# Optimization experiments

Measured on AMD Instinct MI355X. Metric: run time of the kernel, lower is better.

The kernel has to match this reference:

```python
import jax, jax.numpy as jnp
import numpy as np

N = 50000        # nodes
E = 1_600_000    # edges
F_IN = 128       # input feature dim
EMB = 48         # emb_size
HID = 48         # hidden_size
OUT = 64         # out_sizes[0]
K = 7            # Chebyshev order


def setup_inputs() -> dict:
    key = jax.random.key(0)
    ks = jax.random.split(key, 8)
    x = jax.random.normal(ks[0], (N, F_IN), dtype=jnp.float32)
    edge_index = jax.random.randint(ks[1], (2, E), 0, N, dtype=jnp.int32)
    edge_weight = jax.random.uniform(ks[2], (E,), dtype=jnp.float32)
    W_in = jax.random.normal(ks[3], (F_IN, EMB), jnp.float32) / np.float32(np.sqrt(F_IN))
    b_in = jnp.zeros((EMB,), jnp.float32)
    W_cheb = jax.random.normal(ks[4], (K, EMB, HID), jnp.float32) / np.float32(np.sqrt(EMB))
    b_cheb = jnp.zeros((HID,), jnp.float32)
    W_out = jax.random.normal(ks[5], (HID, OUT), jnp.float32) / np.float32(np.sqrt(HID))
    b_out = jnp.zeros((OUT,), jnp.float32)
    return dict(x=x, edge_index=edge_index, edge_weight=edge_weight,
                W_in=W_in, b_in=b_in, W_cheb=W_cheb, b_cheb=b_cheb,
                W_out=W_out, b_out=b_out)


def reference(x, edge_index, edge_weight, W_in, b_in, W_cheb, b_cheb, W_out, b_out):
    row, col = edge_index[0], edge_index[1]
    # PyG ChebConv sym normalization with lambda_max=2:
    #   L_hat = 2/lambda_max * (I - D^-1/2 A D^-1/2) - I = -D^-1/2 A D^-1/2
    deg = jax.ops.segment_sum(edge_weight, row, num_segments=N)
    dinv = jnp.where(deg > 0, jax.lax.rsqrt(deg), 0.0)
    norm = -dinv[row] * edge_weight * dinv[col]  # [E]

    # input Linear + ReLU (Dropout is identity at eval)
    xf = jax.nn.relu(x @ W_in + b_in)  # [N, EMB]

    def prop(t):
        # out[i] = sum_{(j->i) in E} norm_e * t[j]
        return jax.ops.segment_sum(norm[:, None] * t[row], col, num_segments=N)

    # Chebyshev recursion: T0 = x, T1 = L_hat x, T_k = 2 L_hat T_{k-1} - T_{k-2}
    Tx0 = xf
    out = Tx0 @ W_cheb[0]
    Tx1 = prop(Tx0)
    out = out + Tx1 @ W_cheb[1]
    for k in range(2, K):
        Tx2 = 2.0 * prop(Tx1) - Tx0
        out = out + Tx2 @ W_cheb[k]
        Tx0, Tx1 = Tx1, Tx2
    out = out + b_cheb

    y = jax.nn.relu(out)          # ReLU after ChebConv (out_drop = identity at eval)
    y = y @ W_out + b_out          # output Linear
    return (y, xf)
```

## Files before the change

### kernel.cpp

```cpp
#include <hip/hip_runtime.h>
#include <hip/hip_fp16.h>

#define N_NODES 50000
#define N_EDGES 1600000
#define F_IN    128
#define EMB     48
#define HID     48
#define OUTF    64
#define KCH     7
#define TPAD    64

#define NR    8
#define RANGE (N_NODES / NR)
#define BPR   64
#define SLICE (N_EDGES / BPR)
#define HTHREADS 512
#define NBLK  ((N_NODES + 255) / 256)
#define NTILES (N_NODES / 16)

typedef __attribute__((ext_vector_type(8))) _Float16 half8;
typedef __attribute__((ext_vector_type(4))) float f32x4;

#define PROP_GATHER_LOOP(TSRC)                                                  \
    {                                                                           \
        int e16 = s + ((e - s) & ~15);                                          \
        for (; p < e16; p += 16) {                                              \
            float ww[16]; uint2 hv[16];                                         \
            _Pragma("unroll")                                                   \
            for (int j = 0; j < 16; ++j) {                                      \
                uint2 er = edges[p + j];                                        \
                ww[j] = __uint_as_float(er.y);                                  \
                hv[j] = *reinterpret_cast<const uint2*>(                        \
                    TSRC + (size_t)er.x * TPAD + 4 * lane);                     \
            }                                                                   \
            _Pragma("unroll")                                                   \
            for (int j = 0; j < 16; ++j) {                                      \
                __half2 h01 = *reinterpret_cast<__half2*>(&hv[j].x);            \
                __half2 h23 = *reinterpret_cast<__half2*>(&hv[j].y);            \
                a0 += ww[j] * __low2float(h01);                                 \
                a1 += ww[j] * __high2float(h01);                                \
                a2 += ww[j] * __low2float(h23);                                 \
                a3 += ww[j] * __high2float(h23);                                \
            }                                                                   \
        }                                                                       \
        int e4b = p + ((e - p) & ~3);                                           \
        for (; p < e4b; p += 4) {                                               \
            float ww[4]; uint2 hv[4];                                           \
            _Pragma("unroll")                                                   \
            for (int j = 0; j < 4; ++j) {                                       \
                uint2 er = edges[p + j];                                        \
                ww[j] = __uint_as_float(er.y);                                  \
                hv[j] = *reinterpret_cast<const uint2*>(                        \
                    TSRC + (size_t)er.x * TPAD + 4 * lane);                     \
            }                                                                   \
            _Pragma("unroll")                                                   \
            for (int j = 0; j < 4; ++j) {                                       \
                __half2 h01 = *reinterpret_cast<__half2*>(&hv[j].x);            \
                __half2 h23 = *reinterpret_cast<__half2*>(&hv[j].y);            \
                a0 += ww[j] * __low2float(h01);                                 \
                a1 += ww[j] * __high2float(h01);                                \
                a2 += ww[j] * __low2float(h23);                                 \
                a3 += ww[j] * __high2float(h23);                                \
            }                                                                   \
        }                                                                       \
        for (; p < e; ++p) {                                                    \
            uint2 er = edges[p];                                                \
            float wv = __uint_as_float(er.y);                                   \
            uint2 hv = *reinterpret_cast<const uint2*>(                         \
                TSRC + (size_t)er.x * TPAD + 4 * lane);                         \
            __half2 h01 = *reinterpret_cast<__half2*>(&hv.x);                   \
            __half2 h23 = *reinterpret_cast<__half2*>(&hv.y);                   \
            a0 += wv * __low2float(h01);                                        \
            a1 += wv * __high2float(h01);                                       \
            a2 += wv * __low2float(h23);                                        \
            a3 += wv * __high2float(h23);                                       \
        }                                                                       \
    }

__global__ __launch_bounds__(HTHREADS) void hist_part_kernel(
    const int* __restrict__ row, const int* __restrict__ col,
    const float* __restrict__ w,
    unsigned short* __restrict__ pc, float* __restrict__ pd)
{
    __shared__ unsigned lc32[RANGE / 2];
    __shared__ float    ld[RANGE];
    int t = threadIdx.x;
    for (int i = t; i < RANGE / 2; i += HTHREADS) lc32[i] = 0u;
    for (int i = t; i < RANGE; i += HTHREADS) ld[i] = 0.f;
    __syncthreads();
    int r = blockIdx.x / BPR;
    int b = blockIdx.x % BPR;
    int base = r * RANGE;
    int lo = b * SLICE;
    for (int e0 = lo + t * 4; e0 < lo + SLICE; e0 += HTHREADS * 4) {
        int4   c4 = *(const int4*)&col[e0];
        int4   r4 = *(const int4*)&row[e0];
        float4 w4 = *(const float4*)&w[e0];
        int ci, ri;
        ci = c4.x - base; if ((unsigned)ci < RANGE) atomicAdd(&lc32[ci >> 1], 1u << ((ci & 1) * 16));
        ri = r4.x - base; if ((unsigned)ri < RANGE) atomicAdd(&ld[ri], w4.x);
        ci = c4.y - base; if ((unsigned)ci < RANGE) atomicAdd(&lc32[ci >> 1], 1u << ((ci & 1) * 16));
        ri = r4.y - base; if ((unsigned)ri < RANGE) atomicAdd(&ld[ri], w4.y);
        ci = c4.z - base; if ((unsigned)ci < RANGE) atomicAdd(&lc32[ci >> 1], 1u << ((ci & 1) * 16));
        ri = r4.z - base; if ((unsigned)ri < RANGE) atomicAdd(&ld[ri], w4.z);
        ci = c4.w - base; if ((unsigned)ci < RANGE) atomicAdd(&lc32[ci >> 1], 1u << ((ci & 1) * 16));
        ri = r4.w - base; if ((unsigned)ri < RANGE) atomicAdd(&ld[ri], w4.w);
    }
    __syncthreads();
    unsigned short* pcb = pc + (size_t)blockIdx.x * RANGE;
    float*          pdb = pd + (size_t)blockIdx.x * RANGE;
    for (int i = t; i < RANGE; i += HTHREADS) {
        pcb[i] = (unsigned short)((lc32[i >> 1] >> ((i & 1) * 16)) & 0xFFFFu);
        pdb[i] = ld[i];
    }
}

__global__ __launch_bounds__(256) void reduce_kernel(
    unsigned short* __restrict__ pc, const float* __restrict__ pd,
    float* __restrict__ dinv, int* __restrict__ off, int* __restrict__ bsum)
{
    int t = threadIdx.x;
    int n = blockIdx.x * 256 + t;
    int c = 0; float d = 0.f;
    if (n < N_NODES) {
        int r = n / RANGE, i = n - r * RANGE;
        size_t base = (size_t)r * BPR * RANGE + i;
        unsigned csum = 0;
        for (int b = 0; b < BPR; ++b) {
            size_t idx = base + (size_t)b * RANGE;
            unsigned x = pc[idx];
            pc[idx] = (unsigned short)csum;
            csum += x;
            d += pd[idx];
        }
        c = (int)csum;
        dinv[n] = d > 0.f ? rsqrtf(d) : 0.f;
    }
    int lane = t & 63, wid = t >> 6;
    int v = c;
    for (int s = 1; s < 64; s <<= 1) {
        int u = __shfl_up(v, s);
        if (lane >= s) v += u;
    }
    __shared__ int ws[4];
    if (lane == 63) ws[wid] = v;
    __syncthreads();
    int wb = 0;
    for (int i = 0; i < 4; ++i) if (i < wid) wb += ws[i];
    int ex = (v - c) + wb;
    if (n < N_NODES) off[n] = ex;
    if (t == 255) bsum[blockIdx.x] = ex + c;
}

__global__ __launch_bounds__(256) void bsum_scan_kernel(
    int* __restrict__ bsum, int* __restrict__ off)
{
    int t = threadIdx.x;
    int orig = (t < NBLK) ? bsum[t] : 0;
    int lane = t & 63, wid = t >> 6;
    int v = orig;
    for (int s = 1; s < 64; s <<= 1) {
        int u = __shfl_up(v, s);
        if (lane >= s) v += u;
    }
    __shared__ int ws[4];
    if (lane == 63) ws[wid] = v;
    __syncthreads();
    int wb = 0;
    for (int i = 0; i < 4; ++i) if (i < wid) wb += ws[i];
    int ex = (v - orig) + wb;
    if (t < NBLK) bsum[t] = ex;
    if (t == NBLK - 1) off[N_NODES] = ex + orig;
}

__global__ __launch_bounds__(256) void add_off_kernel(
    int* __restrict__ off, const int* __restrict__ bsum)
{
    int n = blockIdx.x * 256 + threadIdx.x;
    if (n < N_NODES) off[n] += bsum[n >> 8];
}

__global__ __launch_bounds__(HTHREADS) void scatter_part_kernel(
    const int* __restrict__ row, const int* __restrict__ col,
    const float* __restrict__ w, const float* __restrict__ dinv,
    const int* __restrict__ off, const unsigned short* __restrict__ pc,
    uint2* __restrict__ edges)
{
    __shared__ unsigned lc32[RANGE / 2];
    int t = threadIdx.x;
    for (int i = t; i < RANGE / 2; i += HTHREADS) lc32[i] = 0u;
    __syncthreads();
    int r = blockIdx.x / BPR;
    int b = blockIdx.x % BPR;
    int base = r * RANGE;
    int lo = b * SLICE;
    const unsigned short* pcb = pc + (size_t)blockIdx.x * RANGE;
    for (int e0 = lo + t * 4; e0 < lo + SLICE; e0 += HTHREADS * 4) {
        int4   c4 = *(const int4*)&col[e0];
        int4   r4 = *(const int4*)&row[e0];
        float4 w4 = *(const float4*)&w[e0];
        #pragma unroll
        for (int j = 0; j < 4; ++j) {
            int c  = (j == 0) ? c4.x : (j == 1) ? c4.y : (j == 2) ? c4.z : c4.w;
            int rw = (j == 0) ? r4.x : (j == 1) ? r4.y : (j == 2) ? r4.z : r4.w;
            float we = (j == 0) ? w4.x : (j == 1) ? w4.y : (j == 2) ? w4.z : w4.w;
            int ci = c - base;
            if ((unsigned)ci < RANGE) {
                unsigned old = atomicAdd(&lc32[ci >> 1], 1u << ((ci & 1) * 16));
                unsigned lrank = (old >> ((ci & 1) * 16)) & 0xFFFFu;
                float nr = -dinv[rw] * we * dinv[c];
                int pos = off[c] + (int)pcb[ci] + (int)lrank;
                edges[pos] = make_uint2((unsigned)rw, __float_as_uint(nr));
            }
        }
    }
}

__global__ __launch_bounds__(256) void xf_mfma_kernel(
    const float* __restrict__ x, const float* __restrict__ Win,
    const float* __restrict__ bin, float* __restrict__ xf_out,
    __half* __restrict__ T0h)
{
    __shared__ half8 Wf[3][4][64];
    __shared__ float bs[EMB];
    int t = threadIdx.x;
    for (int idx = t; idx < 3 * 4 * 64; idx += 256) {
        int j = idx >> 8;
        int rem = idx & 255;
        int s = rem >> 6;
        int l = rem & 63;
        int colw = j * 16 + (l & 15);
        int k0 = s * 32 + (l >> 4) * 8;
        half8 v;
        #pragma unroll
        for (int i = 0; i < 8; ++i)
            v[i] = (_Float16)Win[(k0 + i) * EMB + colw];
        Wf[j][s][l] = v;
    }
    if (t < EMB) bs[t] = bin[t];
    __syncthreads();

    int wid = t >> 6, lane = t & 63;
    int nt = blockIdx.x * 4 + wid;
    if (nt >= NTILES) return;
    int n0 = nt * 16;
    int arow = lane & 15, kg = lane >> 4;

    const float* xr = x + (size_t)(n0 + arow) * F_IN + kg * 8;
    half8 a[4];
    #pragma unroll
    for (int s = 0; s < 4; ++s) {
        f32x4 lo = *reinterpret_cast<const f32x4*>(xr + s * 32);
        f32x4 hi = *reinterpret_cast<const f32x4*>(xr + s * 32 + 4);
        half8 av;
        av[0] = (_Float16)lo[0]; av[1] = (_Float16)lo[1];
        av[2] = (_Float16)lo[2]; av[3] = (_Float16)lo[3];
        av[4] = (_Float16)hi[0]; av[5] = (_Float16)hi[1];
        av[6] = (_Float16)hi[2]; av[7] = (_Float16)hi[3];
        a[s] = av;
    }

    f32x4 c0 = {0.f, 0.f, 0.f, 0.f}, c1 = c0, c2 = c0;
    #pragma unroll
    for (int s = 0; s < 4; ++s) {
        c0 = __builtin_amdgcn_mfma_f32_16x16x32_f16(a[s], Wf[0][s][lane], c0, 0, 0, 0);
        c1 = __builtin_amdgcn_mfma_f32_16x16x32_f16(a[s], Wf[1][s][lane], c1, 0, 0, 0);
        c2 = __builtin_amdgcn_mfma_f32_16x16x32_f16(a[s], Wf[2][s][lane], c2, 0, 0, 0);
    }

    int ccol = lane & 15;
    #pragma unroll
    for (int j = 0; j < 3; ++j) {
        int colg = j * 16 + ccol;
        float bias = bs[colg];
        f32x4 cj = (j == 0) ? c0 : (j == 1) ? c1 : c2;
        #pragma unroll
        for (int r = 0; r < 4; ++r) {
            int n = n0 + kg * 4 + r;
            float v = fmaxf(cj[r] + bias, 0.f);
            xf_out[(size_t)n * EMB + colg] = v;
            T0h[(size_t)n * TPAD + colg] = __float2half_rn(v);
        }
    }
    {
        int n = n0 + (lane >> 2);
        int cp = 48 + (lane & 3) * 4;
        *reinterpret_cast<uint2*>(T0h + (size_t)n * TPAD + cp) = make_uint2(0u, 0u);
    }
}

__global__ __launch_bounds__(256) void prop_k1_kernel(
    const int* __restrict__ off, const uint2* __restrict__ edges,
    const __half* __restrict__ T0, __half* __restrict__ T1,
    const float* __restrict__ W0, const float* __restrict__ W1,
    float* __restrict__ out_acc)
{
    __shared__ float W0s[EMB * HID];
    __shared__ float W1s[EMB * HID];
    __shared__ float tdS[16][EMB + 1];
    __shared__ float t0S[16][EMB + 1];
    int t = threadIdx.x;
    for (int i = t; i < EMB * HID; i += 256) { W0s[i] = W0[i]; W1s[i] = W1[i]; }
    __syncthreads();

    int grp = t >> 4, lane = t & 15;
    int g = blockIdx.x * 16 + grp;

    float a0 = 0.f, a1 = 0.f, a2 = 0.f, a3 = 0.f;
    if (lane < 12) {
        int s = off[g], e = off[g + 1];
        int p = s;
        PROP_GATHER_LOOP(T0)
        uint2 tv = *reinterpret_cast<const uint2*>(T0 + (size_t)g * TPAD + 4 * lane);
        __half2 t01 = *reinterpret_cast<__half2*>(&tv.x);
        __half2 t23 = *reinterpret_cast<__half2*>(&tv.y);
        t0S[grp][4 * lane]     = __low2float(t01);
        t0S[grp][4 * lane + 1] = __high2float(t01);
        t0S[grp][4 * lane + 2] = __low2float(t23);
        t0S[grp][4 * lane + 3] = __high2float(t23);
        tdS[grp][4 * lane]     = a0;
        tdS[grp][4 * lane + 1] = a1;
        tdS[grp][4 * lane + 2] = a2;
        tdS[grp][4 * lane + 3] = a3;
    }
    {
        __half2 h01, h23;
        h01.x = __float2half_rn(a0); h01.y = __float2half_rn(a1);
        h23.x = __float2half_rn(a2); h23.y = __float2half_rn(a3);
        uint2 ov;
        ov.x = *reinterpret_cast<unsigned*>(&h01);
        ov.y = *reinterpret_cast<unsigned*>(&h23);
        *reinterpret_cast<uint2*>(T1 + (size_t)g * TPAD + 4 * lane) = ov;
    }

    float o0 = 0.f, o1 = 0.f, o2 = 0.f;
#pragma unroll 8
    for (int c = 0; c < EMB; ++c) {
        float t1v = tdS[grp][c];
        float t0v = t0S[grp][c];
        o0 += t1v * W1s[c * HID + lane]      + t0v * W0s[c * HID + lane];
        o1 += t1v * W1s[c * HID + lane + 16] + t0v * W0s[c * HID + lane + 16];
        o2 += t1v * W1s[c * HID + lane + 32] + t0v * W0s[c * HID + lane + 32];
    }
    float* orow = out_acc + (size_t)g * HID;
    orow[lane]      = o0;
    orow[lane + 16] = o1;
    orow[lane + 32] = o2;
}

__global__ __launch_bounds__(256) void prop_fused_kernel(
    const int* __restrict__ off, const uint2* __restrict__ edges,
    const __half* __restrict__ tsrc, const __half* __restrict__ tprev,
    __half* __restrict__ tdst, const float* __restrict__ Wk,
    float* __restrict__ out_acc)
{
    __shared__ float Ws[EMB * HID];
    __shared__ float tdS[16][EMB + 1];
    int t = threadIdx.x;
    for (int i = t; i < EMB * HID; i += 256) Ws[i] = Wk[i];
    __syncthreads();

    int grp = t >> 4, lane = t & 15;
    int g = blockIdx.x * 16 + grp;

    float a0 = 0.f, a1 = 0.f, a2 = 0.f, a3 = 0.f;
    if (lane < 12) {
        int s = off[g], e = off[g + 1];
        int p = s;
        PROP_GATHER_LOOP(tsrc)
        uint2 tv = *reinterpret_cast<const uint2*>(tprev + (size_t)g * TPAD + 4 * lane);
        __half2 t01 = *reinterpret_cast<__half2*>(&tv.x);
        __half2 t23 = *reinterpret_cast<__half2*>(&tv.y);
        a0 = 2.f * a0 - __low2float(t01);
        a1 = 2.f * a1 - __high2float(t01);
        a2 = 2.f * a2 - __low2float(t23);
        a3 = 2.f * a3 - __high2float(t23);
        tdS[grp][4 * lane]     = a0;
        tdS[grp][4 * lane + 1] = a1;
        tdS[grp][4 * lane + 2] = a2;
        tdS[grp][4 * lane + 3] = a3;
    }
    {
        __half2 h01, h23;
        h01.x = __float2half_rn(a0); h01.y = __float2half_rn(a1);
        h23.x = __float2half_rn(a2); h23.y = __float2half_rn(a3);
        uint2 ov;
        ov.x = *reinterpret_cast<unsigned*>(&h01);
        ov.y = *reinterpret_cast<unsigned*>(&h23);
        *reinterpret_cast<uint2*>(tdst + (size_t)g * TPAD + 4 * lane) = ov;
    }

    float o0 = 0.f, o1 = 0.f, o2 = 0.f;
#pragma unroll 8
    for (int c = 0; c < EMB; ++c) {
        float tv = tdS[grp][c];
        o0 += tv * Ws[c * HID + lane];
        o1 += tv * Ws[c * HID + lane + 16];
        o2 += tv * Ws[c * HID + lane + 32];
    }
    float* orow = out_acc + (size_t)g * HID;
    orow[lane]      += o0;
    orow[lane + 16] += o1;
    orow[lane + 32] += o2;
}

__global__ __launch_bounds__(256) void prop_final_kernel(
    const int* __restrict__ off, const uint2* __restrict__ edges,
    const __half* __restrict__ tsrc, const __half* __restrict__ tprev,
    const float* __restrict__ Wk, const float* __restrict__ out_acc,
    const float* __restrict__ bch, const float* __restrict__ Wout,
    const float* __restrict__ bout, float* __restrict__ y)
{
    __shared__ float Ws[EMB * HID];
    __shared__ float Wo[HID * OUTF];
    __shared__ float tdS[16][EMB + 1];
    __shared__ float vS[16][HID + 1];
    __shared__ float bchS[HID];
    __shared__ float boS[OUTF];
    int t = threadIdx.x;
    for (int i = t; i < EMB * HID; i += 256) Ws[i] = Wk[i];
    for (int i = t; i < HID * OUTF; i += 256) Wo[i] = Wout[i];
    if (t < HID) bchS[t] = bch[t];
    if (t < OUTF) boS[t] = bout[t];
    __syncthreads();

    int grp = t >> 4, lane = t & 15;
    int g = blockIdx.x * 16 + grp;

    float a0 = 0.f, a1 = 0.f, a2 = 0.f, a3 = 0.f;
    if (lane < 12) {
        int s = off[g], e = off[g + 1];
        int p = s;
        PROP_GATHER_LOOP(tsrc)
        uint2 tv = *reinterpret_cast<const uint2*>(tprev + (size_t)g * TPAD + 4 * lane);
        __half2 t01 = *reinterpret_cast<__half2*>(&tv.x);
        __half2 t23 = *reinterpret_cast<__half2*>(&tv.y);
        a0 = 2.f * a0 - __low2float(t01);
        a1 = 2.f * a1 - __high2float(t01);
        a2 = 2.f * a2 - __low2float(t23);
        a3 = 2.f * a3 - __high2float(t23);
        tdS[grp][4 * lane]     = a0;
        tdS[grp][4 * lane + 1] = a1;
        tdS[grp][4 * lane + 2] = a2;
        tdS[grp][4 * lane + 3] = a3;
    }

    float o0 = 0.f, o1 = 0.f, o2 = 0.f;
#pragma unroll 8
    for (int c = 0; c < EMB; ++c) {
        float tv = tdS[grp][c];
        o0 += tv * Ws[c * HID + lane];
        o1 += tv * Ws[c * HID + lane + 16];
        o2 += tv * Ws[c * HID + lane + 32];
    }
    const float* orow = out_acc + (size_t)g * HID;
    vS[grp][lane]      = fmaxf(orow[lane]      + o0 + bchS[lane],      0.f);
    vS[grp][lane + 16] = fmaxf(orow[lane + 16] + o1 + bchS[lane + 16], 0.f);
    vS[grp][lane + 32] = fmaxf(orow[lane + 32] + o2 + bchS[lane + 32], 0.f);

    float y0 = boS[4 * lane], y1 = boS[4 * lane + 1];
    float y2 = boS[4 * lane + 2], y3 = boS[4 * lane + 3];
#pragma unroll 8
    for (int h = 0; h < HID; ++h) {
        float v = vS[grp][h];
        float4 w4 = *reinterpret_cast<const float4*>(&Wo[h * OUTF + 4 * lane]);
        y0 += v * w4.x; y1 += v * w4.y; y2 += v * w4.z; y3 += v * w4.w;
    }
    *reinterpret_cast<float4*>(y + (size_t)g * OUTF + 4 * lane) =
        make_float4(y0, y1, y2, y3);
}

extern "C" void kernel_launch(void* const* d_in, const int* in_sizes, int n_in,
                              void* d_out, int out_size, void* d_ws, size_t ws_size,
                              hipStream_t stream)
{
    const float* x    = (const float*)d_in[0];
    const int*   ei   = (const int*)d_in[1];
    const float* ew   = (const float*)d_in[2];
    const float* Win  = (const float*)d_in[3];
    const float* bin  = (const float*)d_in[4];
    const float* Wch  = (const float*)d_in[5];
    const float* bch  = (const float*)d_in[6];
    const float* Wout = (const float*)d_in[7];
    const float* bout = (const float*)d_in[8];

    const int* row = ei;
    const int* col = ei + N_EDGES;

    float* y_out  = (float*)d_out;
    float* xf_out = (float*)d_out + (size_t)N_NODES * OUTF;

    char* p = (char*)d_ws;
    auto carve = [&](size_t bytes) {
        void* q = p;
        p += (bytes + 255) & ~(size_t)255;
        return q;
    };
    unsigned short* pc = (unsigned short*)carve((size_t)NR * BPR * RANGE * 2);
    float*    pd  = (float*)carve((size_t)NR * BPR * RANGE * 4);
    float*    dinv = (float*)carve(N_NODES * 4);
    int*      off  = (int*)  carve((N_NODES + 1) * 4);
    int*      bsum = (int*)  carve(NBLK * 4);
    uint2*    edges = (uint2*)carve((size_t)N_EDGES * 8);
    float*    out_acc = (float*)carve((size_t)N_NODES * HID * 4);
    __half*   T0h = (__half*)carve((size_t)N_NODES * TPAD * 2);
    __half*   TAh = (__half*)carve((size_t)N_NODES * TPAD * 2);
    __half*   TBh = (__half*)carve((size_t)N_NODES * TPAD * 2);
    __half*   TCh = (__half*)carve((size_t)N_NODES * TPAD * 2);

    hist_part_kernel<<<NR * BPR, HTHREADS, 0, stream>>>(row, col, ew, pc, pd);
    reduce_kernel<<<NBLK, 256, 0, stream>>>(pc, pd, dinv, off, bsum);
    bsum_scan_kernel<<<1, 256, 0, stream>>>(bsum, off);
    add_off_kernel<<<NBLK, 256, 0, stream>>>(off, bsum);
    scatter_part_kernel<<<NR * BPR, HTHREADS, 0, stream>>>(row, col, ew, dinv, off, pc, edges);

    xf_mfma_kernel<<<(NTILES + 3) / 4, 256, 0, stream>>>(x, Win, bin, xf_out, T0h);

    const int prop_grid = NTILES;

    prop_k1_kernel<<<prop_grid, 256, 0, stream>>>(off, edges, T0h, TAh,
                                                  Wch, Wch + EMB * HID, out_acc);
    const __half* A = T0h;
    __half*       B = TAh;
    __half* bufs[3] = {TBh, TCh, TAh};
    for (int k = 2; k < KCH - 1; ++k) {
        __half* C = bufs[(k - 2) % 3];
        prop_fused_kernel<<<prop_grid, 256, 0, stream>>>(off, edges, B, A,
                                                         C, Wch + (size_t)k * EMB * HID, out_acc);
        A = B; B = C;
    }
    prop_final_kernel<<<prop_grid, 256, 0, stream>>>(off, edges, B, A,
                                                     Wch + (size_t)(KCH - 1) * EMB * HID,
                                                     out_acc, bch, Wout, bout, y_out);
}
```

Baseline: 338.7 us.

## Pre-partition edges by source-node range before histogram and CSR scatter

Adds a three-kernel stable partition (count, scan, scatter) that reorders edges into 7 buckets by row>>13 before the existing histogram and CSR-building kernels run. The intent is to make later degree and scatter accesses to the per-row arrays more local, improving cache behaviour. In exchange it adds an extra full pass over the edge arrays, with writes to new row/col/weight buffers and strided scattered stores, plus three extra launches.

```diff
diff --git a/kernel.cpp b/kernel.cpp
--- a/kernel.cpp
+++ b/kernel.cpp
@@ -17,6 +17,12 @@
 #define HTHREADS 512
 #define NBLK  ((N_NODES + 255) / 256)
 #define NTILES (N_NODES / 16)
+
+#define SRSH  13
+#define NSR   7
+#define PNB   256
+#define PNT   256
+#define PTOT  (PNB * PNT)
 
 typedef __attribute__((ext_vector_type(8))) _Float16 half8;
 typedef __attribute__((ext_vector_type(4))) float f32x4;
@@ -77,6 +83,128 @@
         }                                                                       \
     }
 
+__global__ __launch_bounds__(PNT) void part_count_kernel(
+    const int* __restrict__ row, int* __restrict__ bsum7)
+{
+    __shared__ int cnt[NSR];
+    int t = threadIdx.x;
+    if (t < NSR) cnt[t] = 0;
+    __syncthreads();
+    int tid = blockIdx.x * PNT + t;
+    int c0 = 0, c1 = 0, c2 = 0, c3 = 0, c4 = 0, c5 = 0, c6 = 0;
+    for (int i = tid; i < N_EDGES; i += PTOT) {
+        int b = row[i] >> SRSH;
+        c0 += (b == 0); c1 += (b == 1); c2 += (b == 2); c3 += (b == 3);
+        c4 += (b == 4); c5 += (b == 5); c6 += (b == 6);
+    }
+    if (c0) atomicAdd(&cnt[0], c0);
+    if (c1) atomicAdd(&cnt[1], c1);
+    if (c2) atomicAdd(&cnt[2], c2);
+    if (c3) atomicAdd(&cnt[3], c3);
+    if (c4) atomicAdd(&cnt[4], c4);
+    if (c5) atomicAdd(&cnt[5], c5);
+    if (c6) atomicAdd(&cnt[6], c6);
+    __syncthreads();
+    if (t < NSR) bsum7[blockIdx.x * NSR + t] = cnt[t];
+}
+
+__global__ __launch_bounds__(256) void part_scan_kernel(int* __restrict__ bsum7)
+{
+    __shared__ int ws[NSR][4];
+    __shared__ int tot[NSR];
+    int t = threadIdx.x;
+    int lane = t & 63, wid = t >> 6;
+    int myc[NSR], mypre[NSR];
+#pragma unroll
+    for (int b = 0; b < NSR; ++b) myc[b] = bsum7[t * NSR + b];
+#pragma unroll
+    for (int b = 0; b < NSR; ++b) {
+        int v = myc[b];
+        for (int d = 1; d < 64; d <<= 1) {
+            int u = __shfl_up(v, d);
+            if (lane >= d) v += u;
+        }
+        if (lane == 63) ws[b][wid] = v;
+        mypre[b] = v - myc[b];
+    }
+    __syncthreads();
+    if (t == 0) {
+#pragma unroll
+        for (int b = 0; b < NSR; ++b) {
+            int run = 0;
+            for (int i = 0; i < 4; ++i) { int x = ws[b][i]; ws[b][i] = run; run += x; }
+            tot[b] = run;
+        }
+        int run = 0;
+#pragma unroll
+        for (int b = 0; b < NSR; ++b) { int x = tot[b]; tot[b] = run; run += x; }
+    }
+    __syncthreads();
+#pragma unroll
+    for (int b = 0; b < NSR; ++b)
+        bsum7[t * NSR + b] = tot[b] + ws[b][wid] + mypre[b];
+}
+
+__global__ __launch_bounds__(PNT) void part_scatter_kernel(
+    const int* __restrict__ row, const int* __restrict__ col,
+    const float* __restrict__ w, const int* __restrict__ blockoff,
+    int* __restrict__ row2, int* __restrict__ col2, float* __restrict__ w2)
+{
+    __shared__ int ws[NSR][4];
+    int t = threadIdx.x;
+    int tid = blockIdx.x * PNT + t;
+    int lane = t & 63, wid = t >> 6;
+    int c0 = 0, c1 = 0, c2 = 0, c3 = 0, c4 = 0, c5 = 0, c6 = 0;
+    for (int i = tid; i < N_EDGES; i += PTOT) {
+        int b = row[i] >> SRSH;
+        c0 += (b == 0); c1 += (b == 1); c2 += (b == 2); c3 += (b == 3);
+        c4 += (b == 4); c5 += (b == 5); c6 += (b == 6);
+    }
+    int cArr[NSR] = {c0, c1, c2, c3, c4, c5, c6};
+    int pre[NSR];
+#pragma unroll
+    for (int b = 0; b < NSR; ++b) {
+        int v = cArr[b];
+        for (int d = 1; d < 64; d <<= 1) {
+            int u = __shfl_up(v, d);
+            if (lane >= d) v += u;
+        }
+        if (lane == 63) ws[b][wid] = v;
+        pre[b] = v - cArr[b];
+    }
+    __syncthreads();
+    if (t == 0) {
+#pragma unroll
+        for (int b = 0; b < NSR; ++b) {
+            int run = 0;
+            for (int i = 0; i < 4; ++i) { int x = ws[b][i]; ws[b][i] = run; run += x; }
+        }
+    }
+    __syncthreads();
+    int pos0 = blockoff[blockIdx.x * NSR + 0] + ws[0][wid] + pre[0];
+    int pos1 = blockoff[blockIdx.x * NSR + 1] + ws[1][wid] + pre[1];
+    int pos2 = blockoff[blockIdx.x * NSR + 2] + ws[2][wid] + pre[2];
+    int pos3 = blockoff[blockIdx.x * NSR + 3] + ws[3][wid] + pre[3];
+    int pos4 = blockoff[blockIdx.x * NSR + 4] + ws[4][wid] + pre[4];
+    int pos5 = blockoff[blockIdx.x * NSR + 5] + ws[5][wid] + pre[5];
+    int pos6 = blockoff[blockIdx.x * NSR + 6] + ws[6][wid] + pre[6];
+    for (int i = tid; i < N_EDGES; i += PTOT) {
+        int r = row[i];
+        int cl = col[i];
+        float wv = w[i];
+        int b = r >> SRSH;
+        int p;
+        if      (b == 0) p = pos0++;
+        else if (b == 1) p = pos1++;
+        else if (b == 2) p = pos2++;
+        else if (b == 3) p = pos3++;
+        else if (b == 4) p = pos4++;
+        else if (b == 5) p = pos5++;
+        else             p = pos6++;
+        row2[p] = r; col2[p] = cl; w2[p] = wv;
+    }
+}
+
 __global__ __launch_bounds__(HTHREADS) void hist_part_kernel(
     const int* __restrict__ row, const int* __restrict__ col,
     const float* __restrict__ w,
@@ -501,6 +629,10 @@
     float*    dinv = (float*)carve(N_NODES * 4);
     int*      off  = (int*)  carve((N_NODES + 1) * 4);
     int*      bsum = (int*)  carve(NBLK * 4);
+    int*      bsum7 = (int*) carve((size_t)PNB * NSR * 4);
+    int*      row2 = (int*)  carve((size_t)N_EDGES * 4);
+    int*      col2 = (int*)  carve((size_t)N_EDGES * 4);
+    float*    w2   = (float*)carve((size_t)N_EDGES * 4);
     uint2*    edges = (uint2*)carve((size_t)N_EDGES * 8);
     float*    out_acc = (float*)carve((size_t)N_NODES * HID * 4);
     __half*   T0h = (__half*)carve((size_t)N_NODES * TPAD * 2);
@@ -508,11 +640,15 @@
     __half*   TBh = (__half*)carve((size_t)N_NODES * TPAD * 2);
     __half*   TCh = (__half*)carve((size_t)N_NODES * TPAD * 2);
 
-    hist_part_kernel<<<NR * BPR, HTHREADS, 0, stream>>>(row, col, ew, pc, pd);
+    part_count_kernel<<<PNB, PNT, 0, stream>>>(row, bsum7);
+    part_scan_kernel<<<1, 256, 0, stream>>>(bsum7);
+    part_scatter_kernel<<<PNB, PNT, 0, stream>>>(row, col, ew, bsum7, row2, col2, w2);
+
+    hist_part_kernel<<<NR * BPR, HTHREADS, 0, stream>>>(row2, col2, w2, pc, pd);
     reduce_kernel<<<NBLK, 256, 0, stream>>>(pc, pd, dinv, off, bsum);
     bsum_scan_kernel<<<1, 256, 0, stream>>>(bsum, off);
     add_off_kernel<<<NBLK, 256, 0, stream>>>(off, bsum);
-    scatter_part_kernel<<<NR * BPR, HTHREADS, 0, stream>>>(row, col, ew, dinv, off, pc, edges);
+    scatter_part_kernel<<<NR * BPR, HTHREADS, 0, stream>>>(row2, col2, w2, dinv, off, pc, edges);
 
     xf_mfma_kernel<<<(NTILES + 3) / 4, 256, 0, stream>>>(x, Win, bin, xf_out, T0h);
 
```

Result: slower. 432.1 us (+27.5%).

## Record per-edge local ranks in histogram pass and flatten scatter kernel

Applied to the files above, without the earlier changes.

The histogram kernel now stores each edge's within-block rank from its shared-memory atomic into a new rank16 buffer. The scatter pass no longer repeats the per-range shared-memory atomics over all edges eight times. It becomes a flat one-thread-per-4-edges kernel that reads the precomputed rank and the partition prefix count. This cuts the redundant full-edge scans in the scatter stage, at the cost of an extra global rank buffer write and read plus a scattered pc lookup.

```diff
diff --git a/kernel.cpp b/kernel.cpp
--- a/kernel.cpp
+++ b/kernel.cpp
@@ -80,7 +80,8 @@
 __global__ __launch_bounds__(HTHREADS) void hist_part_kernel(
     const int* __restrict__ row, const int* __restrict__ col,
     const float* __restrict__ w,
-    unsigned short* __restrict__ pc, float* __restrict__ pd)
+    unsigned short* __restrict__ pc, float* __restrict__ pd,
+    unsigned short* __restrict__ rank16)
 {
     __shared__ unsigned lc32[RANGE / 2];
     __shared__ float    ld[RANGE];
@@ -96,15 +97,20 @@
         int4   c4 = *(const int4*)&col[e0];
         int4   r4 = *(const int4*)&row[e0];
         float4 w4 = *(const float4*)&w[e0];
-        int ci, ri;
-        ci = c4.x - base; if ((unsigned)ci < RANGE) atomicAdd(&lc32[ci >> 1], 1u << ((ci & 1) * 16));
-        ri = r4.x - base; if ((unsigned)ri < RANGE) atomicAdd(&ld[ri], w4.x);
-        ci = c4.y - base; if ((unsigned)ci < RANGE) atomicAdd(&lc32[ci >> 1], 1u << ((ci & 1) * 16));
-        ri = r4.y - base; if ((unsigned)ri < RANGE) atomicAdd(&ld[ri], w4.y);
-        ci = c4.z - base; if ((unsigned)ci < RANGE) atomicAdd(&lc32[ci >> 1], 1u << ((ci & 1) * 16));
-        ri = r4.z - base; if ((unsigned)ri < RANGE) atomicAdd(&ld[ri], w4.z);
-        ci = c4.w - base; if ((unsigned)ci < RANGE) atomicAdd(&lc32[ci >> 1], 1u << ((ci & 1) * 16));
-        ri = r4.w - base; if ((unsigned)ri < RANGE) atomicAdd(&ld[ri], w4.w);
+        #pragma unroll
+        for (int j = 0; j < 4; ++j) {
+            int c  = (j == 0) ? c4.x : (j == 1) ? c4.y : (j == 2) ? c4.z : c4.w;
+            int rw = (j == 0) ? r4.x : (j == 1) ? r4.y : (j == 2) ? r4.z : r4.w;
+            float we = (j == 0) ? w4.x : (j == 1) ? w4.y : (j == 2) ? w4.z : w4.w;
+            int ci = c - base;
+            if ((unsigned)ci < RANGE) {
+                unsigned sh = (ci & 1) * 16;
+                unsigned old = atomicAdd(&lc32[ci >> 1], 1u << sh);
+                rank16[e0 + j] = (unsigned short)((old >> sh) & 0xFFFFu);
+            }
+            int ri = rw - base;
+            if ((unsigned)ri < RANGE) atomicAdd(&ld[ri], we);
+        }
     }
     __syncthreads();
     unsigned short* pcb = pc + (size_t)blockIdx.x * RANGE;
@@ -180,39 +186,32 @@
     if (n < N_NODES) off[n] += bsum[n >> 8];
 }
 
-__global__ __launch_bounds__(HTHREADS) void scatter_part_kernel(
+__global__ __launch_bounds__(256) void scatter_flat_kernel(
     const int* __restrict__ row, const int* __restrict__ col,
     const float* __restrict__ w, const float* __restrict__ dinv,
     const int* __restrict__ off, const unsigned short* __restrict__ pc,
-    uint2* __restrict__ edges)
-{
-    __shared__ unsigned lc32[RANGE / 2];
-    int t = threadIdx.x;
-    for (int i = t; i < RANGE / 2; i += HTHREADS) lc32[i] = 0u;
-    __syncthreads();
-    int r = blockIdx.x / BPR;
-    int b = blockIdx.x % BPR;
-    int base = r * RANGE;
-    int lo = b * SLICE;
-    const unsigned short* pcb = pc + (size_t)blockIdx.x * RANGE;
-    for (int e0 = lo + t * 4; e0 < lo + SLICE; e0 += HTHREADS * 4) {
-        int4   c4 = *(const int4*)&col[e0];
-        int4   r4 = *(const int4*)&row[e0];
-        float4 w4 = *(const float4*)&w[e0];
-        #pragma unroll
-        for (int j = 0; j < 4; ++j) {
-            int c  = (j == 0) ? c4.x : (j == 1) ? c4.y : (j == 2) ? c4.z : c4.w;
-            int rw = (j == 0) ? r4.x : (j == 1) ? r4.y : (j == 2) ? r4.z : r4.w;
-            float we = (j == 0) ? w4.x : (j == 1) ? w4.y : (j == 2) ? w4.z : w4.w;
-            int ci = c - base;
-            if ((unsigned)ci < RANGE) {
-                unsigned old = atomicAdd(&lc32[ci >> 1], 1u << ((ci & 1) * 16));
-                unsigned lrank = (old >> ((ci & 1) * 16)) & 0xFFFFu;
-                float nr = -dinv[rw] * we * dinv[c];
-                int pos = off[c] + (int)pcb[ci] + (int)lrank;
-                edges[pos] = make_uint2((unsigned)rw, __float_as_uint(nr));
-            }
-        }
+    const unsigned short* __restrict__ rank16, uint2* __restrict__ edges)
+{
+    int tid = blockIdx.x * 256 + threadIdx.x;
+    int e0 = tid * 4;
+    if (e0 >= N_EDGES) return;
+    int b = e0 / SLICE;
+    int4   c4 = *(const int4*)&col[e0];
+    int4   r4 = *(const int4*)&row[e0];
+    float4 w4 = *(const float4*)&w[e0];
+    ushort4 k4 = *(const ushort4*)&rank16[e0];
+    #pragma unroll
+    for (int j = 0; j < 4; ++j) {
+        int c  = (j == 0) ? c4.x : (j == 1) ? c4.y : (j == 2) ? c4.z : c4.w;
+        int rw = (j == 0) ? r4.x : (j == 1) ? r4.y : (j == 2) ? r4.z : r4.w;
+        float we = (j == 0) ? w4.x : (j == 1) ? w4.y : (j == 2) ? w4.z : w4.w;
+        int rk = (j == 0) ? k4.x : (j == 1) ? k4.y : (j == 2) ? k4.z : k4.w;
+        int rg = c / RANGE;
+        int clocal = c - rg * RANGE;
+        int pre = pc[(size_t)(rg * BPR + b) * RANGE + clocal];
+        float nr = -dinv[rw] * we * dinv[c];
+        int pos = off[c] + pre + rk;
+        edges[pos] = make_uint2((unsigned)rw, __float_as_uint(nr));
     }
 }
 
@@ -498,6 +497,7 @@
     };
     unsigned short* pc = (unsigned short*)carve((size_t)NR * BPR * RANGE * 2);
     float*    pd  = (float*)carve((size_t)NR * BPR * RANGE * 4);
+    unsigned short* rank16 = (unsigned short*)carve((size_t)N_EDGES * 2);
     float*    dinv = (float*)carve(N_NODES * 4);
     int*      off  = (int*)  carve((N_NODES + 1) * 4);
     int*      bsum = (int*)  carve(NBLK * 4);
@@ -508,11 +508,12 @@
     __half*   TBh = (__half*)carve((size_t)N_NODES * TPAD * 2);
     __half*   TCh = (__half*)carve((size_t)N_NODES * TPAD * 2);
 
-    hist_part_kernel<<<NR * BPR, HTHREADS, 0, stream>>>(row, col, ew, pc, pd);
+    hist_part_kernel<<<NR * BPR, HTHREADS, 0, stream>>>(row, col, ew, pc, pd, rank16);
     reduce_kernel<<<NBLK, 256, 0, stream>>>(pc, pd, dinv, off, bsum);
     bsum_scan_kernel<<<1, 256, 0, stream>>>(bsum, off);
     add_off_kernel<<<NBLK, 256, 0, stream>>>(off, bsum);
-    scatter_part_kernel<<<NR * BPR, HTHREADS, 0, stream>>>(row, col, ew, dinv, off, pc, edges);
+    scatter_flat_kernel<<<(N_EDGES / 4 + 255) / 256, 256, 0, stream>>>(
+        row, col, ew, dinv, off, pc, rank16, edges);
 
     xf_mfma_kernel<<<(NTILES + 3) / 4, 256, 0, stream>>>(x, Win, bin, xf_out, T0h);
 
```

Result: no change. 340.4 us (+0.5%).
